# Kernel tuning notes

Measured on AMD Instinct MI355X. Metric: run time of the kernel, lower is better.

Reference implementation:

```python
import jax, jax.numpy as jnp
import numpy as np

BN_EPS = 1e-5


def setup_inputs() -> dict:
    key = jax.random.key(0)
    ks = jax.random.split(key, 8)
    B, C, H, W = 8, 512, 48, 48
    P = 64
    s_in = 1.0 / np.sqrt(C)
    s_p = 1.0 / np.sqrt(P)
    return {
        "x": jax.random.normal(ks[0], (B, C, H, W), dtype=jnp.float32),
        "Wq": jax.random.uniform(ks[1], (P, C), jnp.float32, -s_in, s_in),
        "Wk": jax.random.uniform(ks[2], (P, C), jnp.float32, -s_in, s_in),
        "Wv": jax.random.uniform(ks[3], (C, C), jnp.float32, -s_in, s_in),
        "align_w": jax.random.uniform(ks[4], (P,), jnp.float32, -s_p, s_p),
        "Wfc": jax.random.uniform(ks[5], (C, C), jnp.float32, -s_in, s_in),
        "bfc": jax.random.uniform(ks[6], (C,), jnp.float32, -s_in, s_in),
        "gamma": jnp.ones((C,), jnp.float32),
        "beta": jnp.zeros((C,), jnp.float32),
    }


def reference(x, Wq, Wk, Wv, align_w, Wfc, bfc, gamma, beta):
    B, C, H, W = x.shape
    N = H * W
    px = jnp.transpose(x.reshape(B, C, N), (0, 2, 1))  # [B, N, C]

    q = jnp.tanh(px @ Wq.T)  # [B, N, P]
    k = jnp.tanh(px @ Wk.T)  # [B, N, P]
    v = px @ Wv.T            # [B, N, C]

    # align(q_i * k_j) = sum_p q[b,i,p] * k[b,j,p] * align_w[p]
    scores = jnp.einsum('bip,bjp,p->bij', q, k, align_w)  # [B, N, N]
    attn = jax.nn.softmax(scores, axis=2)

    content = px + attn @ v           # [B, N, C]
    content = content @ Wfc.T + bfc   # fc
    c = jnp.transpose(content, (0, 2, 1)).reshape(B, C, H, W)

    # BatchNorm2d in training mode: batch statistics over (B, H, W), biased var
    mean = jnp.mean(c, axis=(0, 2, 3), keepdims=True)
    var = jnp.var(c, axis=(0, 2, 3), keepdims=True)
    g = gamma.reshape(1, C, 1, 1)
    b = beta.reshape(1, C, 1, 1)
    out = g * (c - mean) * jax.lax.rsqrt(var + BN_EPS) + b
    return jax.nn.relu(out)
```

## Files before the change

kernel.cpp:

```cpp
#include <hip/hip_runtime.h>
#include <stdint.h>

#define BB 8
#define CC 512
#define NN 2304
#define NT16 (NN / 16)
#define NT32 (NN / 32)
#define CT32 (CC / 32)
#define NYB 48

typedef float f32x4 __attribute__((ext_vector_type(4)));
typedef short s16x8 __attribute__((ext_vector_type(8)));

__device__ __forceinline__ unsigned short f2bf(float f) {
  union { float f; uint32_t u; } v; v.f = f;
  uint32_t u = v.u;
  return (unsigned short)((u + 0x7FFFu + ((u >> 16) & 1u)) >> 16);
}
__device__ __forceinline__ float bf2f(unsigned short b) {
  union { uint32_t u; float f; } v; v.u = ((uint32_t)b) << 16;
  return v.f;
}


__global__ void k_prep_w(const float* __restrict__ Wq, const float* __restrict__ Wk,
                         const float* __restrict__ Wv, const float* __restrict__ Wfc,
                         unsigned short* __restrict__ wcat_t, unsigned short* __restrict__ wfc_t) {
  int idx = blockIdx.x * 256 + threadIdx.x;
  const int tot_cat = 640 * 512;
  if (idx < tot_cat) {
    int tile = idx >> 9, inner = idx & 511;
    int j = (tile >> 4) * 16 + (inner >> 5);
    int k = (tile & 15) * 32 + (inner & 31);
    float v = (j < 64) ? Wq[j * 512 + k] : ((j < 128) ? Wk[(j - 64) * 512 + k] : Wv[(j - 128) * 512 + k]);
    wcat_t[idx] = f2bf(v);
  } else if (idx < tot_cat + 512 * 512) {
    int i2 = idx - tot_cat;
    int tile = i2 >> 9, inner = i2 & 511;
    int j = (tile >> 4) * 16 + (inner >> 5);
    int k = (tile & 15) * 32 + (inner & 31);
    wfc_t[i2] = f2bf(Wfc[j * 512 + k]);
  }
}

__global__ void k_px(const float* __restrict__ x, unsigned short* __restrict__ px_t) {
  __shared__ float t[32][33];
  int b = blockIdx.x;
  int nb = blockIdx.y * 32;
  int cb = blockIdx.z * 32;
  int lane = threadIdx.x & 31;
  int row = threadIdx.x >> 5;
  const float* xb = x + (size_t)b * CC * NN;
  for (int rr = 0; rr < 4; rr++) {
    int c = cb + row + 8 * rr;
    t[row + 8 * rr][lane] = xb[(size_t)c * NN + nb + lane];
  }
  __syncthreads();
  int rbase = (b * NN + nb) >> 4;
  int ct = cb >> 5;
  for (int rr = 0; rr < 4; rr++) {
    int nl = row + 8 * rr;
    size_t off = ((size_t)(rbase + (nl >> 4)) * CT32 + ct) * 512 + (nl & 15) * 32 + lane;
    px_t[off] = f2bf(t[lane][nl]);
  }
}

__global__ __launch_bounds__(256, 2) void k_qkv(const unsigned short* __restrict__ px_t,
                                                const unsigned short* __restrict__ wcat_t,
                                                const float* __restrict__ align_w,
                                                unsigned short* __restrict__ q_t,
                                                unsigned short* __restrict__ k_t,
                                                unsigned short* __restrict__ v_row) {
  int b = blockIdx.x;
  int nb = blockIdx.y * 64;
  int jb0 = blockIdx.z * 128;
  int tid = threadIdx.x;
  int w = tid >> 6, l = tid & 63, l15 = l & 15, lq = l >> 4;
  int jw = jb0 + 32 * w;
  int loff = l15 * 32 + 8 * lq;
  int rA = (b * NN + nb) >> 4;
  f32x4 acc[4][2];
  for (int mf = 0; mf < 4; mf++) for (int nf = 0; nf < 2; nf++) acc[mf][nf] = (f32x4){0.f, 0.f, 0.f, 0.f};
  for (int kk = 0; kk < 16; kk++) {
    s16x8 a[4], bbf[2];
    for (int mf = 0; mf < 4; mf++)
      a[mf] = *(const s16x8*)(px_t + ((size_t)(rA + mf) * CT32 + kk) * 512 + loff);
    for (int nf = 0; nf < 2; nf++)
      bbf[nf] = *(const s16x8*)(wcat_t + ((size_t)((jw >> 4) + nf) * CT32 + kk) * 512 + loff);
    for (int mf = 0; mf < 4; mf++)
      for (int nf = 0; nf < 2; nf++)
        acc[mf][nf] = __builtin_amdgcn_mfma_f32_16x16x32_bf16(a[mf], bbf[nf], acc[mf][nf], 0, 0, 0);
  }
  for (int mf = 0; mf < 4; mf++)
    for (int nf = 0; nf < 2; nf++)
      for (int r = 0; r < 4; r++) {
        int j = jw + 16 * nf + l15;
        int nl = 4 * lq + r;
        float v = acc[mf][nf][r];
        if (j < 128) { v = tanhf(v); if (j < 64) v *= align_w[j]; }
        unsigned short bv = f2bf(v);
        if (j < 64)
          q_t[((size_t)(rA + mf) * 2 + (j >> 5)) * 512 + nl * 32 + (j & 31)] = bv;
        else if (j < 128) {
          int jj = j - 64;
          k_t[((size_t)(rA + mf) * 2 + (jj >> 5)) * 512 + nl * 32 + (jj & 31)] = bv;
        } else {
          v_row[((size_t)(b * NN) + nb + 16 * mf + nl) * 512 + (j - 128)] = bv;
        }
      }
}

__global__ void k_vt(const unsigned short* __restrict__ v_row, unsigned short* __restrict__ vt_t) {
  __shared__ uint32_t t[32][33];
  int b = blockIdx.x;
  int nb = blockIdx.y * 32;
  int cb = blockIdx.z * 32;
  int lane = threadIdx.x & 31;
  int row = threadIdx.x >> 5;
  const unsigned short* src = v_row + (size_t)b * NN * 512;
  for (int rr = 0; rr < 4; rr++) {
    int n = nb + row + 8 * rr;
    t[row + 8 * rr][lane] = (uint32_t)src[(size_t)n * 512 + cb + lane];
  }
  __syncthreads();
  unsigned short* dst = vt_t + (size_t)b * (CC / 16) * NT32 * 512;
  for (int rr = 0; rr < 4; rr++) {
    int c = cb + row + 8 * rr;
    size_t off = ((size_t)(c >> 4) * NT32 + (nb >> 5)) * 512 + (c & 15) * 32 + lane;
    dst[off] = (unsigned short)t[lane][row + 8 * rr];
  }
}

__global__ __launch_bounds__(256, 3) void k_attn(const unsigned short* __restrict__ q_t,
                                                 const unsigned short* __restrict__ k_t,
                                                 const unsigned short* __restrict__ vt_t,
                                                 unsigned short* __restrict__ px_t ) {
  __shared__ __align__(16) unsigned short e_s[2][48 * 64];
  __shared__ float rs_s[4][48];
  int bid = blockIdx.x;
  int b = bid & 7;
  int ch = ((bid >> 3) & 1) * 256;
  int ib = (bid >> 4) * 48;
  int tid = threadIdx.x;
  int w = tid >> 6, l = tid & 63, l15 = l & 15, lq = l >> 4;
  int c0 = ch + 64 * w;
  int loff = l15 * 32 + 8 * lq;
  int rQ = (b * NN + ib) >> 4;
  int ktb = b * NT16;
  const unsigned short* vb = vt_t + (size_t)b * (CC / 16) * NT32 * 512;

  s16x8 qa[3][2];
  for (int mf = 0; mf < 3; mf++)
    for (int ks = 0; ks < 2; ks++)
      qa[mf][ks] = *(const s16x8*)(q_t + ((size_t)(rQ + mf) * 2 + ks) * 512 + loff);

  f32x4 acc[3][4];
  for (int mf = 0; mf < 3; mf++) for (int nf = 0; nf < 4; nf++) acc[mf][nf] = (f32x4){0.f, 0.f, 0.f, 0.f};
  float rs[3] = {0.f, 0.f, 0.f};

  s16x8 kf0[2], kf1[2];
  for (int ks = 0; ks < 2; ks++)
    kf0[ks] = *(const s16x8*)(k_t + ((size_t)(ktb + w) * 2 + ks) * 512 + loff);

  auto step = [&](int jt, char* ebuf, s16x8 (&kfu)[2], s16x8 (&kfl)[2]) {
    int jtn = (jt < NN / 64 - 1) ? jt + 1 : jt;
    s16x8 vf[2][4];
    for (int ks = 0; ks < 2; ks++)
      for (int nf = 0; nf < 4; nf++)
        vf[ks][nf] = *(const s16x8*)(vb + ((size_t)((c0 >> 4) + nf) * NT32 + jt * 2 + ks) * 512 + loff);
    for (int ks = 0; ks < 2; ks++)
      kfl[ks] = *(const s16x8*)(k_t + ((size_t)(ktb + jtn * 4 + w) * 2 + ks) * 512 + loff);
    f32x4 sc[3];
    for (int mf = 0; mf < 3; mf++) sc[mf] = (f32x4){0.f, 0.f, 0.f, 0.f};
    __builtin_amdgcn_s_setprio(1);
    for (int ks = 0; ks < 2; ks++)
      for (int mf = 0; mf < 3; mf++)
        sc[mf] = __builtin_amdgcn_mfma_f32_16x16x32_bf16(kfu[ks], qa[mf][ks], sc[mf], 0, 0, 0);
    __builtin_amdgcn_s_setprio(0);
    for (int mf = 0; mf < 3; mf++) {
      float e0 = __expf(sc[mf][0]), e1 = __expf(sc[mf][1]);
      float e2 = __expf(sc[mf][2]), e3 = __expf(sc[mf][3]);
      rs[mf] += (e0 + e1) + (e2 + e3);
      uint32_t p0, p1;
      asm("v_cvt_pk_bf16_f32 %0, %1, %2" : "=v"(p0) : "v"(e0), "v"(e1));
      asm("v_cvt_pk_bf16_f32 %0, %1, %2" : "=v"(p1) : "v"(e2), "v"(e3));
      int i_ = 16 * mf + l15;
      int byte = (i_ * 128 + (16 * w + 4 * lq) * 2) ^ ((i_ & 7) << 4);
      uint2 pp; pp.x = p0; pp.y = p1;
      *(uint2*)(ebuf + byte) = pp;
    }
    asm volatile("s_waitcnt lgkmcnt(0)" ::: "memory");
    __builtin_amdgcn_s_barrier();
    __builtin_amdgcn_sched_barrier(0);
    for (int ks = 0; ks < 2; ks++) {
      s16x8 ef[3];
      for (int mf = 0; mf < 3; mf++) {
        int i_ = 16 * mf + l15;
        int byte = (i_ * 128 + 64 * ks + 16 * lq) ^ ((i_ & 7) << 4);
        ef[mf] = *(const s16x8*)((const char*)ebuf + byte);
      }
      __builtin_amdgcn_s_setprio(1);
      for (int nf = 0; nf < 4; nf++)
        for (int mf = 0; mf < 3; mf++)
          acc[mf][nf] = __builtin_amdgcn_mfma_f32_16x16x32_bf16(ef[mf], vf[ks][nf], acc[mf][nf], 0, 0, 0);
      __builtin_amdgcn_s_setprio(0);
    }
  };

  for (int jt = 0; jt < NN / 64; jt += 2) {
    step(jt, (char*)e_s[0], kf0, kf1);
    step(jt + 1, (char*)e_s[1], kf1, kf0);
  }

  for (int mf = 0; mf < 3; mf++) {
    float v = rs[mf];
    v += __shfl_xor(v, 16);
    v += __shfl_xor(v, 32);
    rs[mf] = v;
  }
  if (lq == 0)
    for (int mf = 0; mf < 3; mf++)
      rs_s[w][16 * mf + l15] = rs[mf];
  __syncthreads();
  float inv[3][4];
  for (int mf = 0; mf < 3; mf++)
    for (int r = 0; r < 4; r++) {
      int i = 16 * mf + 4 * lq + r;
      inv[mf][r] = 1.0f / (rs_s[0][i] + rs_s[1][i] + rs_s[2][i] + rs_s[3][i]);
    }
  for (int mf = 0; mf < 3; mf++)
    for (int nf = 0; nf < 4; nf++)
      for (int r = 0; r < 4; r++) {
        int i = 16 * mf + 4 * lq + r;
        int bn = b * NN + ib + i;
        int c = c0 + 16 * nf + l15;
        size_t off = ((size_t)(bn >> 4) * CT32 + (c >> 5)) * 512 + (bn & 15) * 32 + (c & 31);
        px_t[off] = f2bf(bf2f(px_t[off]) + acc[mf][nf][r] * inv[mf][r]);
      }
}

__global__ __launch_bounds__(256, 3) void k_fc(const unsigned short* __restrict__ px_t,
                                               const unsigned short* __restrict__ wfc_t,
                                               const float* __restrict__ bfc,
                                               float* __restrict__ out,
                                               float2* __restrict__ partials) {
  __shared__ float pss[4][32], psq[4][32];
  int cb = blockIdx.x * 32;
  int yb = blockIdx.y;
  int fb = yb * 384;
  int tid = threadIdx.x;
  int w = tid >> 6, l = tid & 63, l15 = l & 15, lq = l >> 4;
  int fw = fb + 96 * w;
  int loff = l15 * 32 + 8 * lq;
  f32x4 acc[2][6];
  for (int mf = 0; mf < 2; mf++) for (int nf = 0; nf < 6; nf++) acc[mf][nf] = (f32x4){0.f, 0.f, 0.f, 0.f};
  for (int kk = 0; kk < 16; kk++) {
    s16x8 a[2], bbf[6];
    for (int mf = 0; mf < 2; mf++)
      a[mf] = *(const s16x8*)(wfc_t + ((size_t)((cb >> 4) + mf) * CT32 + kk) * 512 + loff);
    for (int nf = 0; nf < 6; nf++)
      bbf[nf] = *(const s16x8*)(px_t + ((size_t)((fw >> 4) + nf) * CT32 + kk) * 512 + loff);
    for (int mf = 0; mf < 2; mf++)
      for (int nf = 0; nf < 6; nf++)
        acc[mf][nf] = __builtin_amdgcn_mfma_f32_16x16x32_bf16(a[mf], bbf[nf], acc[mf][nf], 0, 0, 0);
  }
  float s8[2][4], q8[2][4];
  for (int mf = 0; mf < 2; mf++)
    for (int r = 0; r < 4; r++) {
      int c2 = cb + 16 * mf + 4 * lq + r;
      float bias = bfc[c2];
      float s = 0.f, q = 0.f;
      for (int nf = 0; nf < 6; nf++) {
        float v = acc[mf][nf][r] + bias;
        int flat = fw + 16 * nf + l15;
        int b2 = flat / NN;
        int n = flat - b2 * NN;
        out[((size_t)b2 * CC + c2) * NN + n] = v;
        s += v; q += v * v;
      }
      s8[mf][r] = s; q8[mf][r] = q;
    }
  for (int mf = 0; mf < 2; mf++)
    for (int r = 0; r < 4; r++) {
      float s = s8[mf][r], q = q8[mf][r];
      s += __shfl_xor(s, 1); q += __shfl_xor(q, 1);
      s += __shfl_xor(s, 2); q += __shfl_xor(q, 2);
      s += __shfl_xor(s, 4); q += __shfl_xor(q, 4);
      s += __shfl_xor(s, 8); q += __shfl_xor(q, 8);
      s8[mf][r] = s; q8[mf][r] = q;
    }
  if (l15 == 0)
    for (int mf = 0; mf < 2; mf++)
      for (int r = 0; r < 4; r++) {
        int idx = 16 * mf + 4 * lq + r;
        pss[w][idx] = s8[mf][r];
        psq[w][idx] = q8[mf][r];
      }
  __syncthreads();
  if (tid < 32) {
    float s = pss[0][tid] + pss[1][tid] + pss[2][tid] + pss[3][tid];
    float q = psq[0][tid] + psq[1][tid] + psq[2][tid] + psq[3][tid];
    partials[(size_t)(cb + tid) * NYB + yb] = make_float2(s, q);
  }
}

__global__ void k_stats2(const float2* __restrict__ partials, const float* __restrict__ gamma,
                         const float* __restrict__ beta, float2* __restrict__ ab) {
  int c = blockIdx.x * 256 + threadIdx.x;
  if (c >= CC) return;
  float s = 0.f, q = 0.f;
  for (int i = 0; i < NYB; i++) {
    float2 p = partials[(size_t)c * NYB + i];
    s += p.x; q += p.y;
  }
  const float invn = 1.0f / (BB * NN);
  float mean = s * invn;
  float var = q * invn - mean * mean;
  float a = gamma[c] * rsqrtf(var + 1e-5f);
  ab[c] = make_float2(a, beta[c] - mean * a);
}

__global__ void k_bn(float* __restrict__ out, const float2* __restrict__ ab) {
  int idx = blockIdx.x * 256 + threadIdx.x;
  const int total = BB * CC * NN / 4;
  if (idx >= total) return;
  int c = (idx / (NN / 4)) & (CC - 1);
  float2 p = ab[c];
  f32x4 v = ((f32x4*)out)[idx];
  for (int i = 0; i < 4; i++) v[i] = fmaxf(0.f, v[i] * p.x + p.y);
  ((f32x4*)out)[idx] = v;
}

extern "C" void kernel_launch(void* const* d_in, const int* in_sizes, int n_in,
                              void* d_out, int out_size, void* d_ws, size_t ws_size,
                              hipStream_t stream) {
  const float* x = (const float*)d_in[0];
  const float* Wq = (const float*)d_in[1];
  const float* Wk = (const float*)d_in[2];
  const float* Wv = (const float*)d_in[3];
  const float* align_w = (const float*)d_in[4];
  const float* Wfc = (const float*)d_in[5];
  const float* bfc = (const float*)d_in[6];
  const float* gamma = (const float*)d_in[7];
  const float* beta = (const float*)d_in[8];
  float* out = (float*)d_out;

  char* ws = (char*)d_ws;
  const size_t sz_px = (size_t)BB * NN * CC * 2;
  const size_t sz_q = (size_t)BB * NN * 64 * 2;
  const size_t sz_vr = (size_t)BB * NN * CC * 2;
  unsigned short* px_t = (unsigned short*)(ws);
  unsigned short* q_t = (unsigned short*)(ws + sz_px);
  unsigned short* k_t = (unsigned short*)(ws + sz_px + sz_q);
  unsigned short* v_row = (unsigned short*)(ws + sz_px + 2 * sz_q);
  unsigned short* vt_t = (unsigned short*)(ws + sz_px + 2 * sz_q + sz_vr);
  unsigned short* wcat_t = (unsigned short*)(ws + sz_px + 2 * sz_q + 2 * sz_vr);
  unsigned short* wfc_t = (unsigned short*)(ws + sz_px + 2 * sz_q + 2 * sz_vr + 640 * 512 * 2);
  float2* partials = (float2*)(ws + sz_px + 2 * sz_q + 2 * sz_vr + 640 * 512 * 2 + 512 * 512 * 2);
  float2* ab = (float2*)((char*)partials + (size_t)CC * NYB * sizeof(float2));

  k_prep_w<<<(640 * 512 + 512 * 512 + 255) / 256, 256, 0, stream>>>(Wq, Wk, Wv, Wfc, wcat_t, wfc_t);
  k_px<<<dim3(BB, NN / 32, CC / 32), 256, 0, stream>>>(x, px_t);
  k_qkv<<<dim3(BB, NN / 64, 5), 256, 0, stream>>>(px_t, wcat_t, align_w, q_t, k_t, v_row);
  k_vt<<<dim3(BB, NN / 32, CC / 32), 256, 0, stream>>>(v_row, vt_t);
  k_attn<<<768, 256, 0, stream>>>(q_t, k_t, vt_t, px_t);
  k_fc<<<dim3(CC / 32, NYB), 256, 0, stream>>>(px_t, wfc_t, bfc, out, partials);
  k_stats2<<<2, 256, 0, stream>>>(partials, gamma, beta, ab);
  k_bn<<<(BB * CC * NN / 4 + 255) / 256, 256, 0, stream>>>(out, ab);
}
```

Measured before the change: 191.3 us.

## Fuse V transpose into QKV GEMM epilogue and store FC output as bf16

```diff
diff --git a/kernel.cpp b/kernel.cpp
--- a/kernel.cpp
+++ b/kernel.cpp
@@ -20,6 +20,11 @@
 __device__ __forceinline__ float bf2f(unsigned short b) {
   union { uint32_t u; float f; } v; v.u = ((uint32_t)b) << 16;
   return v.f;
+}
+__device__ __forceinline__ uint32_t cvtpk(float lo, float hi) {
+  uint32_t r;
+  asm("v_cvt_pk_bf16_f32 %0, %1, %2" : "=v"(r) : "v"(lo), "v"(hi));
+  return r;
 }
 
 
@@ -70,64 +75,58 @@
                                                 const float* __restrict__ align_w,
                                                 unsigned short* __restrict__ q_t,
                                                 unsigned short* __restrict__ k_t,
-                                                unsigned short* __restrict__ v_row) {
-  int b = blockIdx.x;
-  int nb = blockIdx.y * 64;
-  int jb0 = blockIdx.z * 128;
+                                                unsigned short* __restrict__ vt_t) {
+  int bid = blockIdx.x;
+  int b = bid & 7;
+  int t = bid >> 3;
+  int z = t % 3;
+  int nb = (t / 3) * 64;
   int tid = threadIdx.x;
   int w = tid >> 6, l = tid & 63, l15 = l & 15, lq = l >> 4;
-  int jw = jb0 + 32 * w;
   int loff = l15 * 32 + 8 * lq;
   int rA = (b * NN + nb) >> 4;
-  f32x4 acc[4][2];
-  for (int mf = 0; mf < 4; mf++) for (int nf = 0; nf < 2; nf++) acc[mf][nf] = (f32x4){0.f, 0.f, 0.f, 0.f};
+  int nfmax = (z == 0) ? 2 : 4;
+  int rowB0 = (z == 0) ? 2 * w : 8 + (z - 1) * 16 + 4 * w;
+  f32x4 acc[4][4];
+  for (int mf = 0; mf < 4; mf++) for (int nf = 0; nf < 4; nf++) acc[mf][nf] = (f32x4){0.f, 0.f, 0.f, 0.f};
   for (int kk = 0; kk < 16; kk++) {
-    s16x8 a[4], bbf[2];
+    s16x8 a[4], bbf[4];
     for (int mf = 0; mf < 4; mf++)
       a[mf] = *(const s16x8*)(px_t + ((size_t)(rA + mf) * CT32 + kk) * 512 + loff);
-    for (int nf = 0; nf < 2; nf++)
-      bbf[nf] = *(const s16x8*)(wcat_t + ((size_t)((jw >> 4) + nf) * CT32 + kk) * 512 + loff);
+    for (int nf = 0; nf < 4; nf++)
+      if (nf < nfmax)
+        bbf[nf] = *(const s16x8*)(wcat_t + ((size_t)(rowB0 + nf) * CT32 + kk) * 512 + loff);
+    for (int mf = 0; mf < 4; mf++)
+      for (int nf = 0; nf < 4; nf++)
+        if (nf < nfmax)
+          acc[mf][nf] = __builtin_amdgcn_mfma_f32_16x16x32_bf16(a[mf], bbf[nf], acc[mf][nf], 0, 0, 0);
+  }
+  if (z == 0) {
     for (int mf = 0; mf < 4; mf++)
       for (int nf = 0; nf < 2; nf++)
-        acc[mf][nf] = __builtin_amdgcn_mfma_f32_16x16x32_bf16(a[mf], bbf[nf], acc[mf][nf], 0, 0, 0);
-  }
-  for (int mf = 0; mf < 4; mf++)
-    for (int nf = 0; nf < 2; nf++)
-      for (int r = 0; r < 4; r++) {
-        int j = jw + 16 * nf + l15;
-        int nl = 4 * lq + r;
-        float v = acc[mf][nf][r];
-        if (j < 128) { v = tanhf(v); if (j < 64) v *= align_w[j]; }
-        unsigned short bv = f2bf(v);
-        if (j < 64)
-          q_t[((size_t)(rA + mf) * 2 + (j >> 5)) * 512 + nl * 32 + (j & 31)] = bv;
-        else if (j < 128) {
-          int jj = j - 64;
-          k_t[((size_t)(rA + mf) * 2 + (jj >> 5)) * 512 + nl * 32 + (jj & 31)] = bv;
-        } else {
-          v_row[((size_t)(b * NN) + nb + 16 * mf + nl) * 512 + (j - 128)] = bv;
+        for (int r = 0; r < 4; r++) {
+          int j = 32 * w + 16 * nf + l15;
+          int nl = 4 * lq + r;
+          float v = tanhf(acc[mf][nf][r]);
+          if (w < 2) {
+            v *= align_w[j];
+            q_t[((size_t)(rA + mf) * 2 + w) * 512 + nl * 32 + (j & 31)] = f2bf(v);
+          } else {
+            k_t[((size_t)(rA + mf) * 2 + (w - 2)) * 512 + nl * 32 + (j & 31)] = f2bf(v);
+          }
         }
-      }
-}
-
-__global__ void k_vt(const unsigned short* __restrict__ v_row, unsigned short* __restrict__ vt_t) {
-  __shared__ uint32_t t[32][33];
-  int b = blockIdx.x;
-  int nb = blockIdx.y * 32;
-  int cb = blockIdx.z * 32;
-  int lane = threadIdx.x & 31;
-  int row = threadIdx.x >> 5;
-  const unsigned short* src = v_row + (size_t)b * NN * 512;
-  for (int rr = 0; rr < 4; rr++) {
-    int n = nb + row + 8 * rr;
-    t[row + 8 * rr][lane] = (uint32_t)src[(size_t)n * 512 + cb + lane];
-  }
-  __syncthreads();
-  unsigned short* dst = vt_t + (size_t)b * (CC / 16) * NT32 * 512;
-  for (int rr = 0; rr < 4; rr++) {
-    int c = cb + row + 8 * rr;
-    size_t off = ((size_t)(c >> 4) * NT32 + (nb >> 5)) * 512 + (c & 15) * 32 + lane;
-    dst[off] = (unsigned short)t[lane][row + 8 * rr];
+  } else {
+    unsigned short* vtb = vt_t + (size_t)b * (CC / 16) * NT32 * 512;
+    for (int mf = 0; mf < 4; mf++)
+      for (int nf = 0; nf < 4; nf++) {
+        int c = (z - 1) * 256 + 64 * w + 16 * nf + l15;
+        uint2 pp;
+        pp.x = cvtpk(acc[mf][nf][0], acc[mf][nf][1]);
+        pp.y = cvtpk(acc[mf][nf][2], acc[mf][nf][3]);
+        int nlo = 16 * (mf & 1) + 4 * lq;
+        size_t off = ((size_t)(c >> 4) * NT32 + (nb >> 5) + (mf >> 1)) * 512 + (c & 15) * 32 + nlo;
+        *(uint2*)(vtb + off) = pp;
+      }
   }
 }
 
@@ -181,12 +180,11 @@
       float e0 = __expf(sc[mf][0]), e1 = __expf(sc[mf][1]);
       float e2 = __expf(sc[mf][2]), e3 = __expf(sc[mf][3]);
       rs[mf] += (e0 + e1) + (e2 + e3);
-      uint32_t p0, p1;
-      asm("v_cvt_pk_bf16_f32 %0, %1, %2" : "=v"(p0) : "v"(e0), "v"(e1));
-      asm("v_cvt_pk_bf16_f32 %0, %1, %2" : "=v"(p1) : "v"(e2), "v"(e3));
+      uint2 pp;
+      pp.x = cvtpk(e0, e1);
+      pp.y = cvtpk(e2, e3);
       int i_ = 16 * mf + l15;
       int byte = (i_ * 128 + (16 * w + 4 * lq) * 2) ^ ((i_ & 7) << 4);
-      uint2 pp; pp.x = p0; pp.y = p1;
       *(uint2*)(ebuf + byte) = pp;
     }
     asm volatile("s_waitcnt lgkmcnt(0)" ::: "memory");
@@ -242,11 +240,13 @@
 __global__ __launch_bounds__(256, 3) void k_fc(const unsigned short* __restrict__ px_t,
                                                const unsigned short* __restrict__ wfc_t,
                                                const float* __restrict__ bfc,
-                                               float* __restrict__ out,
+                                               unsigned short* __restrict__ c16,
                                                float2* __restrict__ partials) {
   __shared__ float pss[4][32], psq[4][32];
-  int cb = blockIdx.x * 32;
-  int yb = blockIdx.y;
+  int bid = blockIdx.x;
+  int s_ = bid >> 3;
+  int yb = (bid & 7) + 8 * (s_ % 6);
+  int cb = (s_ / 6) * 32;
   int fb = yb * 384;
   int tid = threadIdx.x;
   int w = tid >> 6, l = tid & 63, l15 = l & 15, lq = l >> 4;
@@ -275,7 +275,7 @@
         int flat = fw + 16 * nf + l15;
         int b2 = flat / NN;
         int n = flat - b2 * NN;
-        out[((size_t)b2 * CC + c2) * NN + n] = v;
+        c16[((size_t)b2 * CC + c2) * NN + n] = f2bf(v);
         s += v; q += v * v;
       }
       s8[mf][r] = s; q8[mf][r] = q;
@@ -320,15 +320,19 @@
   ab[c] = make_float2(a, beta[c] - mean * a);
 }
 
-__global__ void k_bn(float* __restrict__ out, const float2* __restrict__ ab) {
+__global__ void k_bn(const unsigned short* __restrict__ c16, float* __restrict__ out,
+                     const float2* __restrict__ ab) {
   int idx = blockIdx.x * 256 + threadIdx.x;
-  const int total = BB * CC * NN / 4;
+  const int total = BB * CC * NN / 8;
   if (idx >= total) return;
-  int c = (idx / (NN / 4)) & (CC - 1);
+  int c = (idx / (NN / 8)) & (CC - 1);
   float2 p = ab[c];
-  f32x4 v = ((f32x4*)out)[idx];
-  for (int i = 0; i < 4; i++) v[i] = fmaxf(0.f, v[i] * p.x + p.y);
-  ((f32x4*)out)[idx] = v;
+  s16x8 v = ((const s16x8*)c16)[idx];
+  f32x4 o0, o1;
+  for (int i = 0; i < 4; i++) o0[i] = fmaxf(0.f, bf2f((unsigned short)v[i]) * p.x + p.y);
+  for (int i = 0; i < 4; i++) o1[i] = fmaxf(0.f, bf2f((unsigned short)v[4 + i]) * p.x + p.y);
+  ((f32x4*)out)[idx * 2] = o0;
+  ((f32x4*)out)[idx * 2 + 1] = o1;
 }
 
 extern "C" void kernel_launch(void* const* d_in, const int* in_sizes, int n_in,
@@ -352,7 +356,7 @@
   unsigned short* px_t = (unsigned short*)(ws);
   unsigned short* q_t = (unsigned short*)(ws + sz_px);
   unsigned short* k_t = (unsigned short*)(ws + sz_px + sz_q);
-  unsigned short* v_row = (unsigned short*)(ws + sz_px + 2 * sz_q);
+  unsigned short* c16 = (unsigned short*)(ws + sz_px + 2 * sz_q);
   unsigned short* vt_t = (unsigned short*)(ws + sz_px + 2 * sz_q + sz_vr);
   unsigned short* wcat_t = (unsigned short*)(ws + sz_px + 2 * sz_q + 2 * sz_vr);
   unsigned short* wfc_t = (unsigned short*)(ws + sz_px + 2 * sz_q + 2 * sz_vr + 640 * 512 * 2);
@@ -361,10 +365,9 @@
 
   k_prep_w<<<(640 * 512 + 512 * 512 + 255) / 256, 256, 0, stream>>>(Wq, Wk, Wv, Wfc, wcat_t, wfc_t);
   k_px<<<dim3(BB, NN / 32, CC / 32), 256, 0, stream>>>(x, px_t);
-  k_qkv<<<dim3(BB, NN / 64, 5), 256, 0, stream>>>(px_t, wcat_t, align_w, q_t, k_t, v_row);
-  k_vt<<<dim3(BB, NN / 32, CC / 32), 256, 0, stream>>>(v_row, vt_t);
+  k_qkv<<<864, 256, 0, stream>>>(px_t, wcat_t, align_w, q_t, k_t, vt_t);
   k_attn<<<768, 256, 0, stream>>>(q_t, k_t, vt_t, px_t);
-  k_fc<<<dim3(CC / 32, NYB), 256, 0, stream>>>(px_t, wfc_t, bfc, out, partials);
+  k_fc<<<768, 256, 0, stream>>>(px_t, wfc_t, bfc, c16, partials);
   k_stats2<<<2, 256, 0, stream>>>(partials, gamma, beta, ab);
-  k_bn<<<(BB * CC * NN / 4 + 255) / 256, 256, 0, stream>>>(out, ab);
-}
+  k_bn<<<(BB * CC * NN / 8 + 255) / 256, 256, 0, stream>>>(c16, out, ab);
+}
```

Result: faster. 171.2 us (-10.5%).
